# Kernel tuning notes

Measured on AMD Instinct MI355X. Metric: run time of the kernel, lower is better.

The kernel has to match this reference:

```python
import jax, jax.numpy as jnp
import numpy as np

N_NODES = 50000
N_EDGES = 600000
DIM = 128
META_SIZE = 5000  # output_dim / meta_size


def setup_inputs() -> dict:
    key = jax.random.key(0)
    k1, k2, k3, k4 = jax.random.split(key, 4)
    interval = jax.random.uniform(k1, (N_EDGES,), dtype=jnp.float32)
    embedding = jax.random.normal(k2, (N_NODES, DIM), dtype=jnp.float32)
    edge_index = jax.random.randint(k3, (2, N_EDGES), 0, N_NODES, dtype=jnp.int64)
    # learned parameter; original inits to zeros, use small random for a nontrivial test
    params = jax.random.normal(k4, (DIM, 1), dtype=jnp.float32) * 0.01
    return {"interval": interval, "embedding": embedding, "params": params,
            "edge_index": edge_index, "author_num": 40000}


def reference(interval, embedding, params, edge_index, author_num):
    row, col = edge_index[0], edge_index[1]
    theta = (embedding @ params)[col]                   # [E, 1]
    time_decay = jnp.exp(interval[:, None] * theta)      # [E, 1]
    x_j = time_decay * embedding[col]                    # [E, D] gathered messages
    out = jax.ops.segment_sum(x_j, row, num_segments=embedding.shape[0])  # [N, D]
    return out[META_SIZE:META_SIZE + author_num]
```

## Files before the change

kernel.cpp:

```cpp
#include <hip/hip_runtime.h>

#define DIM  128
#define META 5000
#define CAPP 48
#define CAPB 64

typedef float f32x4 __attribute__((ext_vector_type(4)));

__device__ __forceinline__ ushort f2bf(float f) {
    unsigned u = __float_as_uint(f);
    unsigned r = (u + 0x7FFFu + ((u >> 16) & 1u)) >> 16;
    return (ushort)r;
}
__device__ __forceinline__ float bf_lo(unsigned u) { return __uint_as_float(u << 16); }
__device__ __forceinline__ float bf_hi(unsigned u) { return __uint_as_float(u & 0xFFFF0000u); }

__global__ void theta_cvt_kernel(const float* __restrict__ emb,
                                 const float* __restrict__ params,
                                 float* __restrict__ theta,
                                 ushort* __restrict__ embh,
                                 int* __restrict__ counts,
                                 int n_nodes, int author_num) {
    int gid  = blockIdx.x * blockDim.x + threadIdx.x;
    if (gid < author_num) counts[gid] = 0;
    int wid  = gid >> 6;
    int lane = threadIdx.x & 63;
    int half = lane >> 5;
    int l32  = lane & 31;
    int node = wid * 2 + half;
    if (node >= n_nodes) return;

    const float4 e = *reinterpret_cast<const float4*>(&emb[(size_t)node * DIM + l32 * 4]);
    if (embh) {
        ushort4 h; h.x = f2bf(e.x); h.y = f2bf(e.y); h.z = f2bf(e.z); h.w = f2bf(e.w);
        *reinterpret_cast<ushort4*>(&embh[(size_t)node * DIM + l32 * 4]) = h;
    }
    const float4 p = *reinterpret_cast<const float4*>(&params[l32 * 4]);
    float v = e.x * p.x + e.y * p.y + e.z * p.z + e.w * p.w;
    #pragma unroll
    for (int off = 16; off; off >>= 1) v += __shfl_xor(v, off);
    if (l32 == 0) theta[node] = v;
}

__global__ void fill_packed(const int* __restrict__ row_idx,
                            const int* __restrict__ col_idx,
                            const float* __restrict__ interval,
                            const float* __restrict__ theta,
                            int* __restrict__ counts,
                            uint2* __restrict__ recs,
                            int n_edges, int author_num) {
    int e = blockIdx.x * blockDim.x + threadIdx.x;
    if (e >= n_edges) return;
    int r = row_idx[e] - META;
    if (r < 0 || r >= author_num) return;
    int c = col_idx[e];
    float decay = __expf(interval[e] * theta[c]);
    int slot = atomicAdd(&counts[r], 1);
    if (slot < CAPP)
        recs[(size_t)r * CAPP + slot] = make_uint2(__float_as_uint(decay), (unsigned)c);
}

__global__ void gather_packed3(const ushort* __restrict__ embh,
                               const int* __restrict__ counts,
                               const uint2* __restrict__ recs,
                               float* __restrict__ out, int author_num) {
    int wid  = (blockIdx.x * blockDim.x + threadIdx.x) >> 6;
    int lane = threadIdx.x & 63;
    if (wid >= author_num) return;
    int q   = lane >> 4;
    int l16 = lane & 15;

    int deg = counts[wid];
    if (deg > CAPP) deg = CAPP;

    float decay = 0.f; int c = 0;
    if (lane < deg) {
        uint2 rc = recs[(size_t)wid * CAPP + lane];
        decay = __uint_as_float(rc.x);
        c     = (int)rc.y;
    }

    float a0=0,a1=0,a2=0,a3=0,a4=0,a5=0,a6=0,a7=0;
    int d = 0;
    for (; d + 8 <= deg; d += 8) {
        int e0 = d + 2 * q, e1 = e0 + 1;
        float d0 = __shfl(decay, e0);
        float d1 = __shfl(decay, e1);
        int   c0 = __shfl(c, e0);
        int   c1 = __shfl(c, e1);
        uint4 h0 = *reinterpret_cast<const uint4*>(&embh[(size_t)c0 * DIM + l16 * 8]);
        uint4 h1 = *reinterpret_cast<const uint4*>(&embh[(size_t)c1 * DIM + l16 * 8]);
        a0 += d0 * bf_lo(h0.x); a1 += d0 * bf_hi(h0.x);
        a2 += d0 * bf_lo(h0.y); a3 += d0 * bf_hi(h0.y);
        a4 += d0 * bf_lo(h0.z); a5 += d0 * bf_hi(h0.z);
        a6 += d0 * bf_lo(h0.w); a7 += d0 * bf_hi(h0.w);
        a0 += d1 * bf_lo(h1.x); a1 += d1 * bf_hi(h1.x);
        a2 += d1 * bf_lo(h1.y); a3 += d1 * bf_hi(h1.y);
        a4 += d1 * bf_lo(h1.z); a5 += d1 * bf_hi(h1.z);
        a6 += d1 * bf_lo(h1.w); a7 += d1 * bf_hi(h1.w);
    }
    for (; d + 4 <= deg; d += 4) {
        int e0 = d + q;
        float d0 = __shfl(decay, e0);
        int   c0 = __shfl(c, e0);
        uint4 h0 = *reinterpret_cast<const uint4*>(&embh[(size_t)c0 * DIM + l16 * 8]);
        a0 += d0 * bf_lo(h0.x); a1 += d0 * bf_hi(h0.x);
        a2 += d0 * bf_lo(h0.y); a3 += d0 * bf_hi(h0.y);
        a4 += d0 * bf_lo(h0.z); a5 += d0 * bf_hi(h0.z);
        a6 += d0 * bf_lo(h0.w); a7 += d0 * bf_hi(h0.w);
    }
    if (d < deg) {
        int e0 = d + q;
        bool v = e0 < deg;
        int  se = v ? e0 : d;
        float d0 = __shfl(decay, se);
        int   c0 = __shfl(c, se);
        d0 = v ? d0 : 0.f;
        uint4 h0 = *reinterpret_cast<const uint4*>(&embh[(size_t)c0 * DIM + l16 * 8]);
        a0 += d0 * bf_lo(h0.x); a1 += d0 * bf_hi(h0.x);
        a2 += d0 * bf_lo(h0.y); a3 += d0 * bf_hi(h0.y);
        a4 += d0 * bf_lo(h0.z); a5 += d0 * bf_hi(h0.z);
        a6 += d0 * bf_lo(h0.w); a7 += d0 * bf_hi(h0.w);
    }

    a0 += __shfl_xor(a0, 16); a1 += __shfl_xor(a1, 16);
    a2 += __shfl_xor(a2, 16); a3 += __shfl_xor(a3, 16);
    a4 += __shfl_xor(a4, 16); a5 += __shfl_xor(a5, 16);
    a6 += __shfl_xor(a6, 16); a7 += __shfl_xor(a7, 16);
    a0 += __shfl_xor(a0, 32); a1 += __shfl_xor(a1, 32);
    a2 += __shfl_xor(a2, 32); a3 += __shfl_xor(a3, 32);
    a4 += __shfl_xor(a4, 32); a5 += __shfl_xor(a5, 32);
    a6 += __shfl_xor(a6, 32); a7 += __shfl_xor(a7, 32);

    if (q == 0) {
        float* o = &out[(size_t)wid * DIM + l16 * 8];
        f32x4 vA = {a0, a1, a2, a3};
        f32x4 vB = {a4, a5, a6, a7};
        __builtin_nontemporal_store(vA, reinterpret_cast<f32x4*>(o));
        __builtin_nontemporal_store(vB, reinterpret_cast<f32x4*>(o + 4));
    }
}

__global__ void fill_basic(const int* __restrict__ row_idx,
                           int* __restrict__ counts, int* __restrict__ buckets,
                           int n_edges, int author_num) {
    int e = blockIdx.x * blockDim.x + threadIdx.x;
    if (e >= n_edges) return;
    int r = row_idx[e] - META;
    if (r < 0 || r >= author_num) return;
    int slot = atomicAdd(&counts[r], 1);
    if (slot < CAPB) buckets[(size_t)r * CAPB + slot] = e;
}

__global__ void gather_basic(const float* __restrict__ interval,
                             const float* __restrict__ emb,
                             const int* __restrict__ col_idx,
                             const float* __restrict__ theta,
                             const int* __restrict__ counts,
                             const int* __restrict__ buckets,
                             float* __restrict__ out, int author_num) {
    int wid  = (blockIdx.x * blockDim.x + threadIdx.x) >> 6;
    int lane = threadIdx.x & 63;
    if (wid >= author_num) return;
    int deg = counts[wid]; if (deg > CAPB) deg = CAPB;
    float decay = 0.f; int c = 0;
    if (lane < deg) {
        int e = buckets[(size_t)wid * CAPB + lane];
        c     = col_idx[e];
        decay = __expf(interval[e] * theta[c]);
    }
    float2 acc = {0.f, 0.f};
    for (int d = 0; d < deg; ++d) {
        float dd = __shfl(decay, d);
        int   cd = __shfl(c, d);
        const float2 ev = *reinterpret_cast<const float2*>(&emb[(size_t)cd * DIM + lane * 2]);
        acc.x += dd * ev.x; acc.y += dd * ev.y;
    }
    *reinterpret_cast<float2*>(&out[(size_t)wid * DIM + lane * 2]) = acc;
}

static inline size_t a256(size_t x) { return (x + 255) & ~(size_t)255; }

extern "C" void kernel_launch(void* const* d_in, const int* in_sizes, int n_in,
                              void* d_out, int out_size, void* d_ws, size_t ws_size,
                              hipStream_t stream) {
    const float* interval = (const float*)d_in[0];
    const float* emb      = (const float*)d_in[1];
    const float* params   = (const float*)d_in[2];
    const int*   eidx     = (const int*)d_in[3];
    float* out = (float*)d_out;

    int n_edges    = in_sizes[0];
    int n_nodes    = in_sizes[1] / DIM;
    int author_num = out_size / DIM;

    const int* row_idx = eidx;
    const int* col_idx = eidx + n_edges;

    size_t sz_theta  = a256((size_t)n_nodes * 4);
    size_t sz_counts = a256((size_t)author_num * 4);
    size_t sz_recs   = a256((size_t)author_num * CAPP * 8);
    size_t sz_embh   = a256((size_t)n_nodes * DIM * 2);

    char* ws = (char*)d_ws;
    float* theta  = (float*)ws;
    int*   counts = (int*)(ws + sz_theta);
    char*  rest   = ws + sz_theta + sz_counts;
    size_t avail  = ws_size - (sz_theta + sz_counts);

    const int tb = 256;
    int theta_waves   = (n_nodes + 1) / 2;
    int theta_blocks  = (int)(((long long)theta_waves * 64 + tb - 1) / tb);
    int fill_blocks   = (n_edges + tb - 1) / tb;
    int gather_blocks = (int)(((long long)author_num * 64 + tb - 1) / tb);

    if (avail >= sz_recs + sz_embh) {
        uint2*  recs = (uint2*)rest;
        ushort* embh = (ushort*)(rest + sz_recs);
        theta_cvt_kernel<<<theta_blocks, tb, 0, stream>>>(emb, params, theta, embh,
                                                          counts, n_nodes, author_num);
        fill_packed<<<fill_blocks, tb, 0, stream>>>(row_idx, col_idx, interval, theta,
                                                    counts, recs, n_edges, author_num);
        gather_packed3<<<gather_blocks, tb, 0, stream>>>(embh, counts, recs,
                                                         out, author_num);
    } else {
        int* buckets = (int*)rest;
        theta_cvt_kernel<<<theta_blocks, tb, 0, stream>>>(emb, params, theta, nullptr,
                                                          counts, n_nodes, author_num);
        fill_basic<<<fill_blocks, tb, 0, stream>>>(row_idx, counts, buckets,
                                                   n_edges, author_num);
        gather_basic<<<gather_blocks, tb, 0, stream>>>(interval, emb, col_idx, theta,
                                                       counts, buckets, out, author_num);
    }
}
```

Measured before the change: 59.29 us.

## Fuse theta/bf16 conversion with edge bucketing and defer exp to gather

The theta dot-product/bf16 conversion and the edge bucketing now run as independent block ranges of one fused launch, after a small zero-counts kernel. To make them independent, the bucket records store (col, interval) instead of the precomputed decay, and the exp(interval*theta[col]) is computed in the gather kernel. This removes the dependency between the theta and fill stages, so they can overlap. The cost is an extra launch for zeroing counts and an extra theta gather inside the gather kernel. The fallback path gets a separate theta kernel.

```diff
diff --git a/kernel.cpp b/kernel.cpp
--- a/kernel.cpp
+++ b/kernel.cpp
@@ -15,52 +15,52 @@
 __device__ __forceinline__ float bf_lo(unsigned u) { return __uint_as_float(u << 16); }
 __device__ __forceinline__ float bf_hi(unsigned u) { return __uint_as_float(u & 0xFFFF0000u); }
 
-__global__ void theta_cvt_kernel(const float* __restrict__ emb,
-                                 const float* __restrict__ params,
-                                 float* __restrict__ theta,
-                                 ushort* __restrict__ embh,
-                                 int* __restrict__ counts,
-                                 int n_nodes, int author_num) {
-    int gid  = blockIdx.x * blockDim.x + threadIdx.x;
-    if (gid < author_num) counts[gid] = 0;
-    int wid  = gid >> 6;
-    int lane = threadIdx.x & 63;
-    int half = lane >> 5;
-    int l32  = lane & 31;
-    int node = wid * 2 + half;
-    if (node >= n_nodes) return;
-
-    const float4 e = *reinterpret_cast<const float4*>(&emb[(size_t)node * DIM + l32 * 4]);
-    if (embh) {
+__global__ void zero_counts(int* __restrict__ counts, int author_num) {
+    int i = blockIdx.x * blockDim.x + threadIdx.x;
+    if (i < author_num) counts[i] = 0;
+}
+
+__global__ void fused_theta_bucket(const float* __restrict__ emb,
+                                   const float* __restrict__ params,
+                                   float* __restrict__ theta,
+                                   ushort* __restrict__ embh,
+                                   const int* __restrict__ row_idx,
+                                   const int* __restrict__ col_idx,
+                                   const float* __restrict__ interval,
+                                   int* __restrict__ counts,
+                                   uint2* __restrict__ recs,
+                                   int n_nodes, int n_edges, int author_num,
+                                   int theta_blocks) {
+    if ((int)blockIdx.x < theta_blocks) {
+        int gid  = blockIdx.x * blockDim.x + threadIdx.x;
+        int wid  = gid >> 6;
+        int lane = threadIdx.x & 63;
+        int half = lane >> 5;
+        int l32  = lane & 31;
+        int node = wid * 2 + half;
+        if (node >= n_nodes) return;
+        const float4 e = *reinterpret_cast<const float4*>(&emb[(size_t)node * DIM + l32 * 4]);
         ushort4 h; h.x = f2bf(e.x); h.y = f2bf(e.y); h.z = f2bf(e.z); h.w = f2bf(e.w);
         *reinterpret_cast<ushort4*>(&embh[(size_t)node * DIM + l32 * 4]) = h;
-    }
-    const float4 p = *reinterpret_cast<const float4*>(&params[l32 * 4]);
-    float v = e.x * p.x + e.y * p.y + e.z * p.z + e.w * p.w;
-    #pragma unroll
-    for (int off = 16; off; off >>= 1) v += __shfl_xor(v, off);
-    if (l32 == 0) theta[node] = v;
-}
-
-__global__ void fill_packed(const int* __restrict__ row_idx,
-                            const int* __restrict__ col_idx,
-                            const float* __restrict__ interval,
-                            const float* __restrict__ theta,
-                            int* __restrict__ counts,
-                            uint2* __restrict__ recs,
-                            int n_edges, int author_num) {
-    int e = blockIdx.x * blockDim.x + threadIdx.x;
-    if (e >= n_edges) return;
-    int r = row_idx[e] - META;
-    if (r < 0 || r >= author_num) return;
-    int c = col_idx[e];
-    float decay = __expf(interval[e] * theta[c]);
-    int slot = atomicAdd(&counts[r], 1);
-    if (slot < CAPP)
-        recs[(size_t)r * CAPP + slot] = make_uint2(__float_as_uint(decay), (unsigned)c);
+        const float4 p = *reinterpret_cast<const float4*>(&params[l32 * 4]);
+        float v = e.x * p.x + e.y * p.y + e.z * p.z + e.w * p.w;
+        #pragma unroll
+        for (int off = 16; off; off >>= 1) v += __shfl_xor(v, off);
+        if (l32 == 0) theta[node] = v;
+    } else {
+        int e = (blockIdx.x - theta_blocks) * blockDim.x + threadIdx.x;
+        if (e >= n_edges) return;
+        int r = row_idx[e] - META;
+        if (r < 0 || r >= author_num) return;
+        int slot = atomicAdd(&counts[r], 1);
+        if (slot < CAPP)
+            recs[(size_t)r * CAPP + slot] =
+                make_uint2((unsigned)col_idx[e], __float_as_uint(interval[e]));
+    }
 }
 
 __global__ void gather_packed3(const ushort* __restrict__ embh,
+                               const float* __restrict__ theta,
                                const int* __restrict__ counts,
                                const uint2* __restrict__ recs,
                                float* __restrict__ out, int author_num) {
@@ -76,8 +76,8 @@
     float decay = 0.f; int c = 0;
     if (lane < deg) {
         uint2 rc = recs[(size_t)wid * CAPP + lane];
-        decay = __uint_as_float(rc.x);
-        c     = (int)rc.y;
+        c     = (int)rc.x;
+        decay = __expf(__uint_as_float(rc.y) * theta[c]);
     }
 
     float a0=0,a1=0,a2=0,a3=0,a4=0,a5=0,a6=0,a7=0;
@@ -141,6 +141,24 @@
     }
 }
 
+__global__ void theta_basic(const float* __restrict__ emb,
+                            const float* __restrict__ params,
+                            float* __restrict__ theta,
+                            int* __restrict__ counts,
+                            int n_nodes, int author_num) {
+    int gid  = blockIdx.x * blockDim.x + threadIdx.x;
+    if (gid < author_num) counts[gid] = 0;
+    int node = gid >> 6;
+    int lane = threadIdx.x & 63;
+    if (node >= n_nodes) return;
+    const float2 e = *reinterpret_cast<const float2*>(&emb[(size_t)node * DIM + lane * 2]);
+    const float2 p = *reinterpret_cast<const float2*>(&params[lane * 2]);
+    float v = e.x * p.x + e.y * p.y;
+    #pragma unroll
+    for (int off = 32; off; off >>= 1) v += __shfl_xor(v, off);
+    if (lane == 0) theta[node] = v;
+}
+
 __global__ void fill_basic(const int* __restrict__ row_idx,
                            int* __restrict__ counts, int* __restrict__ buckets,
                            int n_edges, int author_num) {
@@ -209,26 +227,28 @@
     size_t avail  = ws_size - (sz_theta + sz_counts);
 
     const int tb = 256;
+    int zero_blocks   = (author_num + tb - 1) / tb;
     int theta_waves   = (n_nodes + 1) / 2;
     int theta_blocks  = (int)(((long long)theta_waves * 64 + tb - 1) / tb);
-    int fill_blocks   = (n_edges + tb - 1) / tb;
+    int bucket_blocks = (n_edges + tb - 1) / tb;
     int gather_blocks = (int)(((long long)author_num * 64 + tb - 1) / tb);
 
     if (avail >= sz_recs + sz_embh) {
         uint2*  recs = (uint2*)rest;
         ushort* embh = (ushort*)(rest + sz_recs);
-        theta_cvt_kernel<<<theta_blocks, tb, 0, stream>>>(emb, params, theta, embh,
-                                                          counts, n_nodes, author_num);
-        fill_packed<<<fill_blocks, tb, 0, stream>>>(row_idx, col_idx, interval, theta,
-                                                    counts, recs, n_edges, author_num);
-        gather_packed3<<<gather_blocks, tb, 0, stream>>>(embh, counts, recs,
+        zero_counts<<<zero_blocks, tb, 0, stream>>>(counts, author_num);
+        fused_theta_bucket<<<theta_blocks + bucket_blocks, tb, 0, stream>>>(
+            emb, params, theta, embh, row_idx, col_idx, interval,
+            counts, recs, n_nodes, n_edges, author_num, theta_blocks);
+        gather_packed3<<<gather_blocks, tb, 0, stream>>>(embh, theta, counts, recs,
                                                          out, author_num);
     } else {
         int* buckets = (int*)rest;
-        theta_cvt_kernel<<<theta_blocks, tb, 0, stream>>>(emb, params, theta, nullptr,
-                                                          counts, n_nodes, author_num);
-        fill_basic<<<fill_blocks, tb, 0, stream>>>(row_idx, counts, buckets,
-                                                   n_edges, author_num);
+        int tb_blocks = (n_nodes * 64 + tb - 1) / tb;
+        theta_basic<<<tb_blocks, tb, 0, stream>>>(emb, params, theta, counts,
+                                                  n_nodes, author_num);
+        fill_basic<<<bucket_blocks, tb, 0, stream>>>(row_idx, counts, buckets,
+                                                     n_edges, author_num);
         gather_basic<<<gather_blocks, tb, 0, stream>>>(interval, emb, col_idx, theta,
                                                        counts, buckets, out, author_num);
     }
```

Result: slower. 68.55 us (+15.6%).
